# Kernel optimization log

Measured on AMD Instinct MI355X. Metric: run time of the kernel, lower is better.

Reference implementation:

```python
import jax, jax.numpy as jnp
import numpy as np

IN_DIM = 512        # cfg.hidden_channels
NUM_H_PATCH = 16    # cfg.num_h_patch (v_dim); also k dim after split
BASE = 10000.0      # cfg.base
OUT_DIM = IN_DIM * 2 * NUM_H_PATCH


def setup_inputs() -> dict:
    key = jax.random.key(0)
    k1, k2, k3 = jax.random.split(key, 3)
    b, n = 16, 256
    token = jax.random.normal(k1, (b, n, IN_DIM), dtype=jnp.float32)
    W_proj = jax.random.normal(k2, (IN_DIM, OUT_DIM), dtype=jnp.float32) * (IN_DIM ** -0.5)
    b_proj = jax.random.normal(k3, (OUT_DIM,), dtype=jnp.float32) * 0.01
    return {"token": token, "W_proj": W_proj, "b_proj": b_proj}


def reference(token, W_proj, b_proj):
    b, n, _ = token.shape
    d = 2 * NUM_H_PATCH
    kv = token @ W_proj + b_proj                       # [b, n, in_dim*2*num_h_patch]
    kv = kv.reshape(b, n, IN_DIM, d).transpose(0, 2, 1, 3)  # b h n d, h=in_dim
    k = kv[..., : NUM_H_PATCH]                         # [b, h, n, num_h_patch]
    v = kv[..., NUM_H_PATCH:]                          # [b, h, n, num_h_patch]
    k = jax.nn.silu(k)
    # rotary phase: theta buffer (h, 1, num_h_patch//2), index = n-1-arange(n)
    d_theta = IN_DIM * NUM_H_PATCH
    freqs = BASE ** (-2.0 / d_theta * jnp.arange(d_theta // 2, dtype=jnp.float32))
    theta = freqs.reshape(IN_DIM, 1, NUM_H_PATCH // 2)
    index = (n - 1 - jnp.arange(n, dtype=jnp.float32)).reshape(n, 1)
    ang = theta * index                                # [h, n, num_h_patch//2]
    ang = jnp.repeat(ang, 2, axis=-1)                  # '... d -> ... (d g)', g=2
    cos, sin = jnp.cos(ang), jnp.sin(ang)
    # rotate-half: interleave (-k_odd, k_even)
    k_half = jnp.stack([-k[..., 1::2], k[..., ::2]], axis=-1).reshape(k.shape)
    k = k * cos + k_half * sin
    # fast-weight memory: per-head outer-product reduction over sequence
    wm = jnp.einsum('bhnd,bhne->bdeh', k, v)           # [b, num_h_patch, num_h_patch, in_dim]
    return wm.reshape(b, NUM_H_PATCH * NUM_H_PATCH, IN_DIM)
```

## Files before the change

### kernel.cpp

```cpp
#include <hip/hip_runtime.h>
#include <hip/hip_bf16.h>

typedef __bf16 bf16;
typedef __bf16 bf16x4 __attribute__((ext_vector_type(4)));
typedef __bf16 bf16x8 __attribute__((ext_vector_type(8)));
typedef float f32x4 __attribute__((ext_vector_type(4)));

#define GLOBAL_AS __attribute__((address_space(1)))
#define LDS_AS __attribute__((address_space(3)))

__device__ __forceinline__ void gload_lds16(const void* g, void* l) {
  __builtin_amdgcn_global_load_lds((const GLOBAL_AS void*)g, (LDS_AS void*)l, 16, 0, 0);
}

__global__ __launch_bounds__(256) void cvt_token_k(const float* __restrict__ t,
                                                   bf16* __restrict__ o) {
  int base = (blockIdx.x * 256 + threadIdx.x) * 4;
  f32x4 v = *(const f32x4*)(t + base);
  bf16x4 b;
  b[0] = (bf16)v[0]; b[1] = (bf16)v[1]; b[2] = (bf16)v[2]; b[3] = (bf16)v[3];
  *(bf16x4*)(o + base) = b;
}

__global__ __launch_bounds__(256) void transpose_w_k(const float* __restrict__ w,
                                                     bf16* __restrict__ wt) {
  __shared__ float tile[32][33];
  int j0 = blockIdx.x * 32;
  int k0 = blockIdx.y * 32;
  int tx = threadIdx.x & 31;
  int ty = threadIdx.x >> 5;
#pragma unroll
  for (int i = 0; i < 4; ++i)
    tile[ty + i * 8][tx] = w[(size_t)(k0 + ty + i * 8) * 16384 + j0 + tx];
  __syncthreads();
#pragma unroll
  for (int i = 0; i < 4; ++i)
    wt[(size_t)(j0 + ty + i * 8) * 512 + k0 + tx] = (bf16)tile[tx][ty + i * 8];
}

__global__ __launch_bounds__(512, 2) void fused_main_k(
    const bf16* __restrict__ A, const bf16* __restrict__ Wt,
    const float* __restrict__ bias, float* __restrict__ out) {
  __shared__ char smem[65536];
  const int tid = threadIdx.x;
  const int lane = tid & 63;
  const int w = tid >> 6;
  const int wr = w >> 1;
  const int wc = w & 1;
  const int b = blockIdx.y;
  const int hg = blockIdx.x;
  const int m0 = b << 8;
  const int j0 = hg << 7;

  f32x4 acc[4][4] = {};

  for (int ks = 0; ks < 8; ++ks) {
    const int kbase = ks << 6;
#pragma unroll
    for (int i = 0; i < 4; ++i) {
      int q = (i * 8 + w) * 64 + lane;
      int r = q >> 3;
      int cc = (q & 7) ^ (r & 7);
      gload_lds16(A + (size_t)(m0 + r) * 512 + kbase + cc * 8,
                  smem + (i * 8 + w) * 1024);
    }
#pragma unroll
    for (int i = 0; i < 2; ++i) {
      int q = (i * 8 + w) * 64 + lane;
      int r = q >> 3;
      int cc = (q & 7) ^ (r & 7);
      gload_lds16(Wt + (size_t)(j0 + r) * 512 + kbase + cc * 8,
                  smem + 32768 + (i * 8 + w) * 1024);
    }
    __syncthreads();
#pragma unroll
    for (int kk = 0; kk < 2; ++kk) {
      const int cbyte = (kk * 32 + (lane >> 4) * 8) * 2;
      bf16x8 af[4], bfr[4];
#pragma unroll
      for (int mf = 0; mf < 4; ++mf) {
        int r = wr * 64 + mf * 16 + (lane & 15);
        af[mf] = *(const bf16x8*)(smem + r * 128 + (cbyte ^ ((r & 7) << 4)));
      }
#pragma unroll
      for (int nf = 0; nf < 4; ++nf) {
        int r = wc * 64 + nf * 16 + (lane & 15);
        bfr[nf] = *(const bf16x8*)(smem + 32768 + r * 128 + (cbyte ^ ((r & 7) << 4)));
      }
#pragma unroll
      for (int mf = 0; mf < 4; ++mf)
#pragma unroll
        for (int nf = 0; nf < 4; ++nf)
          acc[mf][nf] = __builtin_amdgcn_mfma_f32_16x16x32_bf16(
              af[mf], bfr[nf], acc[mf][nf], 0, 0, 0);
    }
    __syncthreads();
  }

#pragma unroll
  for (int nf = 0; nf < 4; ++nf) {
    const int col = wc * 64 + nf * 16 + (lane & 15);
    const int hl = col >> 5;
    const int dd = lane & 15;
    const bool isk = ((nf & 1) == 0);
    const float bv = bias[j0 + col];
    float freq = 0.f, sgn = 0.f;
    if (isk) {
      const int t = dd >> 1;
      const int hglob = (hg << 2) + hl;
      freq = exp2f((float)(hglob * 8 + t) * (-13.287712379549449f / 4096.0f));
      sgn = (dd & 1) ? 1.0f : -1.0f;
    }
#pragma unroll
    for (int mf = 0; mf < 4; ++mf) {
      const int n0 = wr * 64 + mf * 16 + ((lane >> 4) << 2);
      f32x4 c = acc[mf][nf];
#pragma unroll
      for (int j = 0; j < 4; ++j) {
        float x = c[j] + bv;
        if (isk) x = x * __builtin_amdgcn_rcpf(1.0f + __expf(-x));
        c[j] = x;
      }
      if (isk) {
#pragma unroll
        for (int j = 0; j < 4; ++j) {
          float partner = __shfl_xor(c[j], 1);
          float sv, cv;
          __sincosf(freq * (float)(255 - (n0 + j)), &sv, &cv);
          c[j] = c[j] * cv + sgn * partner * sv;
        }
      }
      bf16x4 pk;
      pk[0] = (bf16)c[0]; pk[1] = (bf16)c[1]; pk[2] = (bf16)c[2]; pk[3] = (bf16)c[3];
      int byte = (isk ? 0 : 32768) + hl * 8192 + dd * 512 + n0 * 2;
      byte ^= ((dd & 7) << 4);
      *(bf16x4*)(smem + byte) = pk;
    }
  }
  __syncthreads();

  {
    const int hl = w >> 1;
    const int half = w & 1;
    const int dd = lane & 15;
    f32x4 d2 = {0.f, 0.f, 0.f, 0.f};
#pragma unroll
    for (int kk = 0; kk < 4; ++kk) {
      const int n0 = half * 128 + kk * 32 + ((lane >> 4) << 3);
      int byte = hl * 8192 + dd * 512 + n0 * 2;
      byte ^= ((dd & 7) << 4);
      bf16x8 ka = *(const bf16x8*)(smem + byte);
      bf16x8 vb = *(const bf16x8*)(smem + 32768 + byte);
      d2 = __builtin_amdgcn_mfma_f32_16x16x32_bf16(ka, vb, d2, 0, 0, 0);
    }
    __syncthreads();
    float* part = (float*)smem;
#pragma unroll
    for (int j = 0; j < 4; ++j) {
      int de = (((lane >> 4) << 2) + j) * 16 + dd;
      part[w * 256 + de] = d2[j];
    }
  }
  __syncthreads();

  if (tid < 256) {
    const float* part = (const float*)smem;
    f32x4 o;
#pragma unroll
    for (int hl = 0; hl < 4; ++hl)
      o[hl] = part[(2 * hl) * 256 + tid] + part[(2 * hl + 1) * 256 + tid];
    *(f32x4*)(out + (size_t)b * 131072 + (size_t)tid * 512 + hg * 4) = o;
  }
}

extern "C" void kernel_launch(void* const* d_in, const int* in_sizes, int n_in,
                              void* d_out, int out_size, void* d_ws, size_t ws_size,
                              hipStream_t stream) {
  const float* token = (const float*)d_in[0];
  const float* W     = (const float*)d_in[1];
  const float* bias  = (const float*)d_in[2];
  float* out = (float*)d_out;

  bf16* Abf = (bf16*)d_ws;
  bf16* Wt  = (bf16*)((char*)d_ws + (size_t)4 * 1024 * 1024);

  cvt_token_k<<<2048, 256, 0, stream>>>(token, Abf);
  transpose_w_k<<<dim3(512, 16), 256, 0, stream>>>(W, Wt);
  fused_main_k<<<dim3(128, 16), 512, 0, stream>>>(Abf, Wt, bias, out);
}
```

Before: 93.99 us.

## Pre-pack operands into MFMA fragment layout and pipeline A staging triple-buffered

The conversion kernels now write A and B in MFMA fragment order. The main GEMM then loads B fragments straight from global memory into registers, double-buffered, and streams A through a three-slot LDS ring using async global-to-LDS loads with explicit vmcnt waits. A single barrier per k-step replaces the two syncthreads, the k-step shrinks to 32, occupancy hints rise to 4 blocks, and MFMA issue priority is raised. The aim is to overlap memory with MFMA and cut LDS traffic and barrier stalls, at the cost of more register pressure and fragile hand-tuned wait counts.

```diff
diff --git a/kernel.cpp b/kernel.cpp
--- a/kernel.cpp
+++ b/kernel.cpp
@@ -12,34 +12,50 @@
 __device__ __forceinline__ void gload_lds16(const void* g, void* l) {
   __builtin_amdgcn_global_load_lds((const GLOBAL_AS void*)g, (LDS_AS void*)l, 16, 0, 0);
 }
-
-__global__ __launch_bounds__(256) void cvt_token_k(const float* __restrict__ t,
-                                                   bf16* __restrict__ o) {
-  int base = (blockIdx.x * 256 + threadIdx.x) * 4;
-  f32x4 v = *(const f32x4*)(t + base);
-  bf16x4 b;
-  b[0] = (bf16)v[0]; b[1] = (bf16)v[1]; b[2] = (bf16)v[2]; b[3] = (bf16)v[3];
-  *(bf16x4*)(o + base) = b;
-}
-
-__global__ __launch_bounds__(256) void transpose_w_k(const float* __restrict__ w,
-                                                     bf16* __restrict__ wt) {
-  __shared__ float tile[32][33];
-  int j0 = blockIdx.x * 32;
-  int k0 = blockIdx.y * 32;
-  int tx = threadIdx.x & 31;
-  int ty = threadIdx.x >> 5;
-#pragma unroll
-  for (int i = 0; i < 4; ++i)
-    tile[ty + i * 8][tx] = w[(size_t)(k0 + ty + i * 8) * 16384 + j0 + tx];
+#define WAITV(n) asm volatile("s_waitcnt vmcnt(" #n ")" ::: "memory")
+
+__global__ __launch_bounds__(256) void pack_a_k(const float* __restrict__ t,
+                                                bf16* __restrict__ o) {
+  int g = blockIdx.x * 4 + (threadIdx.x >> 6);
+  int lane = threadIdx.x & 63;
+  int mf = g & 3, wr = (g >> 2) & 3, kb = (g >> 4) & 15, b = g >> 8;
+  int m = (b << 8) + (wr << 6) + (mf << 4) + (lane & 15);
+  int k = (kb << 5) + ((lane >> 4) << 3);
+  const float* src = t + (size_t)m * 512 + k;
+  f32x4 v0 = *(const f32x4*)src;
+  f32x4 v1 = *(const f32x4*)(src + 4);
+  bf16x8 p;
+  p[0] = (bf16)v0[0]; p[1] = (bf16)v0[1]; p[2] = (bf16)v0[2]; p[3] = (bf16)v0[3];
+  p[4] = (bf16)v1[0]; p[5] = (bf16)v1[1]; p[6] = (bf16)v1[2]; p[7] = (bf16)v1[3];
+  *(bf16x8*)(o + ((size_t)g << 9) + (lane << 3)) = p;
+}
+
+__global__ __launch_bounds__(256) void pack_b_k(const float* __restrict__ wsrc,
+                                                bf16* __restrict__ o) {
+  __shared__ float tile[32][65];
+  int tileid = blockIdx.x;
+  int kb = tileid & 15, jg = tileid >> 4;
+  int k0 = kb << 5, j0 = jg << 6;
+  int tid = threadIdx.x;
+  {
+    int r = tid >> 3, c8 = (tid & 7) << 3;
+    const float* src = wsrc + (size_t)(k0 + r) * 16384 + j0 + c8;
+    f32x4 a = *(const f32x4*)src;
+    f32x4 b2 = *(const f32x4*)(src + 4);
+    *(f32x4*)&tile[r][c8] = a;
+    *(f32x4*)&tile[r][c8 + 4] = b2;
+  }
   __syncthreads();
-#pragma unroll
-  for (int i = 0; i < 4; ++i)
-    wt[(size_t)(j0 + ty + i * 8) * 512 + k0 + tx] = (bf16)tile[tx][ty + i * 8];
-}
-
-__global__ __launch_bounds__(512, 2) void fused_main_k(
-    const bf16* __restrict__ A, const bf16* __restrict__ Wt,
+  int lr = tid & 15, khi = (tid >> 4) & 3, nf = tid >> 6;
+  int j = (nf << 4) + lr, kk = khi << 3;
+  bf16x8 p;
+#pragma unroll
+  for (int e = 0; e < 8; ++e) p[e] = (bf16)tile[kk + e][j];
+  *(bf16x8*)(o + ((size_t)(((jg << 4) + kb) * 4 + nf) << 9) + ((tid & 63) << 3)) = p;
+}
+
+__global__ __launch_bounds__(512, 4) void fused_main_k(
+    const bf16* __restrict__ Ap, const bf16* __restrict__ Bp,
     const float* __restrict__ bias, float* __restrict__ out) {
   __shared__ char smem[65536];
   const int tid = threadIdx.x;
@@ -49,53 +65,59 @@
   const int wc = w & 1;
   const int b = blockIdx.y;
   const int hg = blockIdx.x;
-  const int m0 = b << 8;
   const int j0 = hg << 7;
 
+  const bf16* Abase = Ap + ((size_t)(b * 16) << 13);
+  const bf16* Bbase = Bp + ((size_t)((hg * 2 + wc) * 16) << 11);
+
   f32x4 acc[4][4] = {};
-
-  for (int ks = 0; ks < 8; ++ks) {
-    const int kbase = ks << 6;
-#pragma unroll
-    for (int i = 0; i < 4; ++i) {
-      int q = (i * 8 + w) * 64 + lane;
-      int r = q >> 3;
-      int cc = (q & 7) ^ (r & 7);
-      gload_lds16(A + (size_t)(m0 + r) * 512 + kbase + cc * 8,
-                  smem + (i * 8 + w) * 1024);
-    }
-#pragma unroll
-    for (int i = 0; i < 2; ++i) {
-      int q = (i * 8 + w) * 64 + lane;
-      int r = q >> 3;
-      int cc = (q & 7) ^ (r & 7);
-      gload_lds16(Wt + (size_t)(j0 + r) * 512 + kbase + cc * 8,
-                  smem + 32768 + (i * 8 + w) * 1024);
-    }
-    __syncthreads();
-#pragma unroll
-    for (int kk = 0; kk < 2; ++kk) {
-      const int cbyte = (kk * 32 + (lane >> 4) * 8) * 2;
-      bf16x8 af[4], bfr[4];
-#pragma unroll
-      for (int mf = 0; mf < 4; ++mf) {
-        int r = wr * 64 + mf * 16 + (lane & 15);
-        af[mf] = *(const bf16x8*)(smem + r * 128 + (cbyte ^ ((r & 7) << 4)));
-      }
-#pragma unroll
-      for (int nf = 0; nf < 4; ++nf) {
-        int r = wc * 64 + nf * 16 + (lane & 15);
-        bfr[nf] = *(const bf16x8*)(smem + 32768 + r * 128 + (cbyte ^ ((r & 7) << 4)));
-      }
-#pragma unroll
-      for (int mf = 0; mf < 4; ++mf)
-#pragma unroll
-        for (int nf = 0; nf < 4; ++nf)
-          acc[mf][nf] = __builtin_amdgcn_mfma_f32_16x16x32_bf16(
-              af[mf], bfr[nf], acc[mf][nf], 0, 0, 0);
-    }
-    __syncthreads();
-  }
+  bf16x8 bfA[4], bfB[4];
+
+#define LOAD_BFR(dst_, kb_) do { \
+    const bf16* p_ = Bbase + ((kb_) * 2048) + (lane << 3); \
+    dst_[0] = *(const bf16x8*)(p_);        \
+    dst_[1] = *(const bf16x8*)(p_ + 512);  \
+    dst_[2] = *(const bf16x8*)(p_ + 1024); \
+    dst_[3] = *(const bf16x8*)(p_ + 1536); \
+  } while (0)
+#define STAGE_A(kb_, buf_) do { \
+    gload_lds16(Abase + ((size_t)(kb_) << 13) + (tid << 3), \
+                smem + (buf_) * 16384 + tid * 16); \
+    gload_lds16(Abase + ((size_t)(kb_) << 13) + ((tid + 512) << 3), \
+                smem + (buf_) * 16384 + (tid + 512) * 16); \
+  } while (0)
+
+  LOAD_BFR(bfA, 0);
+  STAGE_A(0, 0);
+  STAGE_A(1, 1);
+  WAITV(2);
+  __builtin_amdgcn_s_barrier();
+  asm volatile("" ::: "memory");
+
+#pragma unroll
+  for (int t = 0; t < 16; ++t) {
+    const int cb = (t % 3) * 16384;
+    if (t < 15) { if (t & 1) LOAD_BFR(bfA, t + 1); else LOAD_BFR(bfB, t + 1); }
+    if (t < 14) STAGE_A(t + 2, (t + 2) % 3);
+    bf16x8 af[4];
+#pragma unroll
+    for (int mf = 0; mf < 4; ++mf)
+      af[mf] = *(const bf16x8*)(smem + cb + ((wr * 4 + mf) << 10) + (lane << 4));
+    __builtin_amdgcn_s_setprio(1);
+#pragma unroll
+    for (int mf = 0; mf < 4; ++mf)
+#pragma unroll
+      for (int nf = 0; nf < 4; ++nf)
+        acc[mf][nf] = __builtin_amdgcn_mfma_f32_16x16x32_bf16(
+            af[mf], (t & 1) ? bfB[nf] : bfA[nf], acc[mf][nf], 0, 0, 0);
+    __builtin_amdgcn_s_setprio(0);
+    asm volatile("" ::: "memory");
+    if (t < 14) { WAITV(2); } else { WAITV(0); }
+    __builtin_amdgcn_s_barrier();
+    asm volatile("" ::: "memory");
+  }
+#undef LOAD_BFR
+#undef STAGE_A
 
 #pragma unroll
   for (int nf = 0; nf < 4; ++nf) {
@@ -106,9 +128,9 @@
     const float bv = bias[j0 + col];
     float freq = 0.f, sgn = 0.f;
     if (isk) {
-      const int t = dd >> 1;
+      const int tp = dd >> 1;
       const int hglob = (hg << 2) + hl;
-      freq = exp2f((float)(hglob * 8 + t) * (-13.287712379549449f / 4096.0f));
+      freq = exp2f((float)(hglob * 8 + tp) * (-13.287712379549449f / 4096.0f));
       sgn = (dd & 1) ? 1.0f : -1.0f;
     }
 #pragma unroll
@@ -181,10 +203,10 @@
   const float* bias  = (const float*)d_in[2];
   float* out = (float*)d_out;
 
-  bf16* Abf = (bf16*)d_ws;
-  bf16* Wt  = (bf16*)((char*)d_ws + (size_t)4 * 1024 * 1024);
-
-  cvt_token_k<<<2048, 256, 0, stream>>>(token, Abf);
-  transpose_w_k<<<dim3(512, 16), 256, 0, stream>>>(W, Wt);
-  fused_main_k<<<dim3(128, 16), 512, 0, stream>>>(Abf, Wt, bias, out);
-}
+  bf16* Apack = (bf16*)d_ws;
+  bf16* Bpack = (bf16*)((char*)d_ws + (size_t)4 * 1024 * 1024);
+
+  pack_a_k<<<1024, 256, 0, stream>>>(token, Apack);
+  pack_b_k<<<4096, 256, 0, stream>>>(W, Bpack);
+  fused_main_k<<<dim3(128, 16), 512, 0, stream>>>(Apack, Bpack, bias, out);
+}
```

Measured after the change: 96.35 us. 1.03x slower.
